# Performance work log

Hardware: AMD Instinct MI355X
Metric: run time of the kernel (lower is better)

Reference implementation:

```python
import jax, jax.numpy as jnp
import numpy as np
from jax import lax

EPS = 1e-5
NF, NH, HD = 1024, 2, 2  # num_features, heads, head_size (hidden_size=4)


def _prelu(x, a):
    return jnp.where(x >= 0, x, a * x)


def _bn2d(x, g, b):  # training-mode BatchNorm2d over (N,H,W)
    m = x.mean(axis=(0, 2, 3), keepdims=True)
    v = ((x - m) ** 2).mean(axis=(0, 2, 3), keepdims=True)
    return (x - m) / jnp.sqrt(v + EPS) * g[None, :, None, None] + b[None, :, None, None]


def _bn1d(x, g, b):  # training-mode BatchNorm1d over batch
    m = x.mean(axis=0, keepdims=True)
    v = ((x - m) ** 2).mean(axis=0, keepdims=True)
    return (x - m) / jnp.sqrt(v + EPS) * g + b


def _ln(x, g, b):
    m = x.mean(axis=-1, keepdims=True)
    v = ((x - m) ** 2).mean(axis=-1, keepdims=True)
    return (x - m) / jnp.sqrt(v + EPS) * g + b


def _conv(x, w, b, stride):
    y = lax.conv_general_dilated(x, w, window_strides=stride, padding='VALID',
                                 dimension_numbers=('NCHW', 'OIHW', 'NCHW'))
    return y + b[None, :, None, None]


def setup_inputs() -> dict:
    key = jax.random.key(0)
    ks = jax.random.split(key, 24)
    r = lambda i, shape, s=0.05: jax.random.normal(ks[i], shape, jnp.float32) * s
    ones = lambda n: jnp.ones((n,), jnp.float32)
    zeros = lambda n: jnp.zeros((n,), jnp.float32)
    return {
        'vertex_pos': r(0, (32, 3), 1.0),
        'body_mesh': r(1, (32, 20813, 3), 1.0),
        'conv1_w': r(2, (3, 1, 409, 3)), 'conv1_b': r(3, (3,)),
        'bn1_g': ones(3), 'bn1_b': zeros(3),
        'conv2_w': r(4, (3, 1, 330, 3)), 'conv2_b': r(5, (3,)),
        'bn2_g': ones(3), 'bn2_b': zeros(3),
        'prelu_a': jnp.float32(0.25),
        'wq': r(6, (4, 9)), 'bq': r(7, (4,)),
        'wk': r(8, (4, 9)), 'bk': r(9, (4,)),
        'wv': r(10, (4, 9)), 'bv': r(11, (4,)),
        'fc_w': r(12, (1024, 4096)), 'fc_b': r(13, (1024,)),
        'ff1_w': r(14, (1024, 1024)), 'ff1_b': r(15, (1024,)),
        'ln_g': ones(1024), 'ln_b': zeros(1024),
        'ff2_w': r(16, (48, 1024)), 'ff2_b': r(17, (48,)),
        'fus_w0': r(18, (48, 32, 3)), 'fus_b0': r(19, (48, 32)),
        'fus_w1': r(20, (48, 128, 32)), 'fus_b1': r(21, (48, 128)),
        'bnf0_g': ones(32), 'bnf0_b': zeros(32),
        'bnf1_g': ones(128), 'bnf1_b': zeros(128),
        'prelu_f': jnp.float32(0.25),
        'out_w': r(22, (1, 128)), 'out_b': r(23, (1,)),
    }


def reference(vertex_pos, body_mesh, conv1_w, conv1_b, bn1_g, bn1_b, conv2_w, conv2_b,
              bn2_g, bn2_b, prelu_a, wq, bq, wk, bk, wv, bv, fc_w, fc_b,
              ff1_w, ff1_b, ln_g, ln_b, ff2_w, ff2_b,
              fus_w0, fus_b0, fus_w1, fus_b1, bnf0_g, bnf0_b, bnf1_g, bnf1_b,
              prelu_f, out_w, out_b):
    B = vertex_pos.shape[0]
    # --- mesh encoder (MultiHeadAttention_conv.mesh_encoder) ---
    mesh = body_mesh.reshape(B, 1, -1, 3)                             # [B,1,20813,3]
    x = _bn2d(_conv(mesh, conv1_w, conv1_b, (6, 1)), bn1_g, bn1_b)    # [B,3,3401,1]
    x = x.reshape(B, 1, -1, 3)                                        # [B,1,3401,3]
    x = _bn2d(_conv(x, conv2_w, conv2_b, (1, 1)), bn2_g, bn2_b)       # [B,3,3072,1]
    x = _prelu(x.reshape(B, NF, -1), prelu_a)                         # [B,1024,9]
    # --- multi-head attention ---
    def heads(t):  # [B,NF,NH*HD] -> [B,NH,NF,HD]
        return t.reshape(B, NF, NH, HD).transpose(0, 2, 1, 3)
    q = heads(x @ wq.T + bq)
    k = heads(x @ wk.T + bk)
    v = heads(x @ wv.T + bv)
    scores = jnp.einsum('bhqd,bhkd->bhqk', q, k) / (HD ** 0.5)        # [B,2,1024,1024]
    attn = jax.nn.softmax(scores, axis=-1)
    av = jnp.einsum('bhqk,bhkd->bhqd', attn, v)
    av = av.transpose(0, 2, 1, 3).reshape(B, NF * NH * HD)            # [B,4096]
    h = av @ fc_w.T + fc_b                                            # [B,1024]
    # --- GMW feed-forward (residual) + motion weights ---
    h = h + jax.nn.elu(_ln(h @ ff1_w.T + ff1_b, ln_g, ln_b))
    mw = h @ ff2_w.T + ff2_b                                          # [B,48]
    w = mw / jnp.sum(mw, axis=1, keepdims=True)                       # normalized gates
    # --- fused MoE stage: 48 experts per depth, batched as one grouped GEMM ---
    s = vertex_pos.reshape(B, 3)
    for We, be, g, bb in ((fus_w0, fus_b0, bnf0_g, bnf0_b),
                          (fus_w1, fus_b1, bnf1_g, bnf1_b)):
        y = jnp.einsum('eoi,bi->beo', We, s) + be[None]               # [B,48,out]
        s = jnp.einsum('beo,be->bo', y, w)                            # gated sum over experts
        s = _prelu(_bn1d(s, g, bb), prelu_f)
    return jax.nn.sigmoid(s @ out_w.T + out_b)                        # [B,1]
```

## Files before the change

### kernel.cpp

```cpp
#include <hip/hip_runtime.h>

#define EPSF 1e-5f

__device__ __forceinline__ float wred(float v) {
#pragma unroll
  for (int off = 32; off > 0; off >>= 1) v += __shfl_down(v, off, 64);
  return v;
}

__global__ __launch_bounds__(256) void k_conv1(
    const float* __restrict__ mesh, const float* __restrict__ cw,
    const float* __restrict__ cb, float* __restrict__ out,
    float* __restrict__ part) {
  __shared__ float wsm[3684];
  __shared__ float sm[3513];
  __shared__ float red[3072];
  __shared__ float pm2[384];
  __shared__ float redm[4][6];
  const int tid = threadIdx.x;
  const int tile = blockIdx.x % 27, b = blockIdx.x / 27;
  const int oh0 = tile << 7;
  const int nvalid = min(128, 3401 - oh0);
  const int nload = (nvalid - 1) * 18 + 1227;
  for (int j = tid; j < 3681; j += 256) {
    int c = (j >= 2454) ? 2 : ((j >= 1227) ? 1 : 0);
    wsm[c * 1228 + (j - c * 1227)] = cw[j];
  }
  const float* src = mesh + b * 62439 + oh0 * 18;
  for (int j = tid; j < nload; j += 256) sm[j] = src[j];
  __syncthreads();
  const int kc = tid >> 5, s = tid & 31;
  const int i0 = kc * 154, i1 = min(1227, i0 + 154);
  float acc[4][3] = {};
  const float* xb = sm + s * 18;
  int i = i0;
#pragma unroll 2
  for (; i + 1 < i1; i += 2) {
    float2 w0 = *(const float2*)(wsm + i);
    float2 w1 = *(const float2*)(wsm + 1228 + i);
    float2 w2 = *(const float2*)(wsm + 2456 + i);
#pragma unroll
    for (int r = 0; r < 4; ++r) {
      float2 x = *(const float2*)(xb + r * 576 + i);
      acc[r][0] = fmaf(w0.x, x.x, fmaf(w0.y, x.y, acc[r][0]));
      acc[r][1] = fmaf(w1.x, x.x, fmaf(w1.y, x.y, acc[r][1]));
      acc[r][2] = fmaf(w2.x, x.x, fmaf(w2.y, x.y, acc[r][2]));
    }
  }
  if (i < i1) {
    float w0 = wsm[i], w1 = wsm[1228 + i], w2 = wsm[2456 + i];
#pragma unroll
    for (int r = 0; r < 4; ++r) {
      float x = xb[r * 576 + i];
      acc[r][0] = fmaf(w0, x, acc[r][0]);
      acc[r][1] = fmaf(w1, x, acc[r][1]);
      acc[r][2] = fmaf(w2, x, acc[r][2]);
    }
  }
#pragma unroll
  for (int r = 0; r < 4; ++r)
#pragma unroll
    for (int ch = 0; ch < 3; ++ch)
      red[kc * 384 + s * 12 + r * 3 + ch] = acc[r][ch];
  __syncthreads();
  float v0 = cb[tid % 3];
#pragma unroll
  for (int c2 = 0; c2 < 8; ++c2) v0 += red[c2 * 384 + tid];
  pm2[tid] = v0;
  if (tid < 128) {
    float v1 = cb[(tid + 256) % 3];
#pragma unroll
    for (int c2 = 0; c2 < 8; ++c2) v1 += red[c2 * 384 + tid + 256];
    pm2[tid + 256] = v1;
  }
  __syncthreads();
  float st[6] = {0.f, 0.f, 0.f, 0.f, 0.f, 0.f};
  if (tid < 128 && tid < nvalid) {
    const int s2 = tid & 31, r2 = tid >> 5;
    float y0 = pm2[s2 * 12 + r2 * 3 + 0];
    float y1 = pm2[s2 * 12 + r2 * 3 + 1];
    float y2 = pm2[s2 * 12 + r2 * 3 + 2];
    float* op = out + b * 10203 + oh0 + tid;
    op[0] = y0; op[3401] = y1; op[6802] = y2;
    st[0] = y0; st[1] = y0 * y0; st[2] = y1; st[3] = y1 * y1; st[4] = y2; st[5] = y2 * y2;
  }
  const int lane = tid & 63, wid = tid >> 6;
#pragma unroll
  for (int c = 0; c < 6; ++c) {
    float rv = wred(st[c]);
    if (lane == 0) redm[wid][c] = rv;
  }
  __syncthreads();
  if (tid < 6)
    part[tid * 864 + blockIdx.x] = redm[0][tid] + redm[1][tid] + redm[2][tid] + redm[3][tid];
}

__global__ __launch_bounds__(256) void k_conv2(
    const float* __restrict__ x1, const float* __restrict__ part1,
    const float* __restrict__ g1, const float* __restrict__ be1,
    const float* __restrict__ cw, const float* __restrict__ cb,
    float* __restrict__ out, float* __restrict__ part) {
  __shared__ float wT[3024];
  __shared__ float P[3][852];
  __shared__ float red[1536];
  __shared__ float redm[4][6];
  __shared__ float coef[6];
  const int tid = threadIdx.x;
  const int lane = tid & 63, wid = tid >> 6;
  {
    float r6[6] = {0.f, 0.f, 0.f, 0.f, 0.f, 0.f};
    for (int j = tid; j < 864; j += 256) {
#pragma unroll
      for (int c = 0; c < 6; ++c) r6[c] += part1[c * 864 + j];
    }
#pragma unroll
    for (int c = 0; c < 6; ++c) {
      float rv = wred(r6[c]);
      if (lane == 0) redm[wid][c] = rv;
    }
    __syncthreads();
    if (tid == 0) {
      const float inv_n = 1.f / (32.f * 3401.f);
#pragma unroll
      for (int c = 0; c < 3; ++c) {
        float s = redm[0][2 * c] + redm[1][2 * c] + redm[2][2 * c] + redm[3][2 * c];
        float ss = redm[0][2 * c + 1] + redm[1][2 * c + 1] + redm[2][2 * c + 1] + redm[3][2 * c + 1];
        float m = s * inv_n;
        float var = ss * inv_n - m * m;
        float a = g1[c] * rsqrtf(var + EPSF);
        coef[c] = a; coef[3 + c] = be1[c] - m * a;
      }
    }
  }
  for (int j = tid; j < 3024; j += 256) {
    int u = j / 1008, rem = j - u * 1008;
    int c = rem / 336, t = rem - c * 336;
    wT[j] = (t < 330) ? cw[c * 990 + 3 * t + u] : 0.f;
  }
  __syncthreads();
  const int tile = blockIdx.x % 6, b = blockIdx.x / 6;
  const int oh0 = tile << 9;
  const int zbase = oh0 * 3;
  const float* src = x1 + b * 10203 + zbase;
  for (int j = tid; j < 2556; j += 256) {
    int rel = j / 3, u = j - rel * 3;
    float val = 0.f;
    int z = zbase + j;
    if (z <= 10202) {
      int c = (z >= 6802) ? 2 : ((z >= 3401) ? 1 : 0);
      val = fmaf(coef[c], src[j], coef[3 + c]);
    }
    P[u][rel] = val;
  }
  __syncthreads();
  const int kc = tid >> 7, s = tid & 127;
  const int t0 = kc * 168;
  const int xb = s << 2;
  float acc0[4] = {}, acc1[4] = {}, acc2[4] = {};
  float4 cur0 = *(const float4*)&P[0][xb + t0];
  float4 cur1 = *(const float4*)&P[1][xb + t0];
  float4 cur2 = *(const float4*)&P[2][xb + t0];
  float4 nxt0 = *(const float4*)&P[0][xb + t0 + 4];
  float4 nxt1 = *(const float4*)&P[1][xb + t0 + 4];
  float4 nxt2 = *(const float4*)&P[2][xb + t0 + 4];
  const int tend = t0 + 168;
  for (int tg = t0; tg < tend; tg += 4) {
#define CONV2_U(ACC0, ACC1, ACC2, UOFF, CUR, NXT)                                                  \
    {                                                                                              \
      const float* wu = wT + UOFF + tg;                                                            \
      float2 wa0 = *(const float2*)(wu);                                                           \
      float2 wb0 = *(const float2*)(wu + 2);                                                       \
      float2 wa1 = *(const float2*)(wu + 336);                                                     \
      float2 wb1 = *(const float2*)(wu + 338);                                                     \
      float2 wa2 = *(const float2*)(wu + 672);                                                     \
      float2 wb2 = *(const float2*)(wu + 674);                                                     \
      float x0 = CUR.x, x1v = CUR.y, x2v = CUR.z, x3v = CUR.w;                                     \
      float x4 = NXT.x, x5 = NXT.y, x6 = NXT.z;                                                    \
      ACC0[0] = fmaf(wa0.x, x0,  fmaf(wa0.y, x1v, fmaf(wb0.x, x2v, fmaf(wb0.y, x3v, ACC0[0]))));  \
      ACC0[1] = fmaf(wa0.x, x1v, fmaf(wa0.y, x2v, fmaf(wb0.x, x3v, fmaf(wb0.y, x4,  ACC0[1]))));  \
      ACC0[2] = fmaf(wa0.x, x2v, fmaf(wa0.y, x3v, fmaf(wb0.x, x4,  fmaf(wb0.y, x5,  ACC0[2]))));  \
      ACC0[3] = fmaf(wa0.x, x3v, fmaf(wa0.y, x4,  fmaf(wb0.x, x5,  fmaf(wb0.y, x6,  ACC0[3]))));  \
      ACC1[0] = fmaf(wa1.x, x0,  fmaf(wa1.y, x1v, fmaf(wb1.x, x2v, fmaf(wb1.y, x3v, ACC1[0]))));  \
      ACC1[1] = fmaf(wa1.x, x1v, fmaf(wa1.y, x2v, fmaf(wb1.x, x3v, fmaf(wb1.y, x4,  ACC1[1]))));  \
      ACC1[2] = fmaf(wa1.x, x2v, fmaf(wa1.y, x3v, fmaf(wb1.x, x4,  fmaf(wb1.y, x5,  ACC1[2]))));  \
      ACC1[3] = fmaf(wa1.x, x3v, fmaf(wa1.y, x4,  fmaf(wb1.x, x5,  fmaf(wb1.y, x6,  ACC1[3]))));  \
      ACC2[0] = fmaf(wa2.x, x0,  fmaf(wa2.y, x1v, fmaf(wb2.x, x2v, fmaf(wb2.y, x3v, ACC2[0]))));  \
      ACC2[1] = fmaf(wa2.x, x1v, fmaf(wa2.y, x2v, fmaf(wb2.x, x3v, fmaf(wb2.y, x4,  ACC2[1]))));  \
      ACC2[2] = fmaf(wa2.x, x2v, fmaf(wa2.y, x3v, fmaf(wb2.x, x4,  fmaf(wb2.y, x5,  ACC2[2]))));  \
      ACC2[3] = fmaf(wa2.x, x3v, fmaf(wa2.y, x4,  fmaf(wb2.x, x5,  fmaf(wb2.y, x6,  ACC2[3]))));  \
    }
    CONV2_U(acc0, acc1, acc2, 0,    cur0, nxt0)
    CONV2_U(acc0, acc1, acc2, 1008, cur1, nxt1)
    CONV2_U(acc0, acc1, acc2, 2016, cur2, nxt2)
#undef CONV2_U
    cur0 = nxt0; cur1 = nxt1; cur2 = nxt2;
    nxt0 = *(const float4*)&P[0][xb + tg + 8];
    nxt1 = *(const float4*)&P[1][xb + tg + 8];
    nxt2 = *(const float4*)&P[2][xb + tg + 8];
  }
  if (kc == 1) {
#pragma unroll
    for (int r = 0; r < 4; ++r) {
      red[s * 12 + r] = acc0[r];
      red[s * 12 + 4 + r] = acc1[r];
      red[s * 12 + 8 + r] = acc2[r];
    }
  }
  __syncthreads();
  float st[6] = {0.f, 0.f, 0.f, 0.f, 0.f, 0.f};
  if (kc == 0) {
    float y0[4], y1[4], y2[4];
#pragma unroll
    for (int r = 0; r < 4; ++r) {
      y0[r] = acc0[r] + red[s * 12 + r] + cb[0];
      y1[r] = acc1[r] + red[s * 12 + 4 + r] + cb[1];
      y2[r] = acc2[r] + red[s * 12 + 8 + r] + cb[2];
      st[0] += y0[r]; st[1] += y0[r] * y0[r];
      st[2] += y1[r]; st[3] += y1[r] * y1[r];
      st[4] += y2[r]; st[5] += y2[r] * y2[r];
    }
    float* op = out + b * 9216 + oh0 + xb;
    *(float4*)(op)        = make_float4(y0[0], y0[1], y0[2], y0[3]);
    *(float4*)(op + 3072) = make_float4(y1[0], y1[1], y1[2], y1[3]);
    *(float4*)(op + 6144) = make_float4(y2[0], y2[1], y2[2], y2[3]);
  }
#pragma unroll
  for (int c = 0; c < 6; ++c) {
    float rv = wred(st[c]);
    if (lane == 0) redm[wid][c] = rv;
  }
  __syncthreads();
  if (tid < 6)
    part[tid * 192 + blockIdx.x] = redm[0][tid] + redm[1][tid] + redm[2][tid] + redm[3][tid];
}

__global__ __launch_bounds__(256) void k_qkv(
    const float* __restrict__ x2, const float* __restrict__ part2,
    const float* __restrict__ g2, const float* __restrict__ be2,
    const float* __restrict__ pa_p,
    const float* __restrict__ wq, const float* __restrict__ bq,
    const float* __restrict__ wk, const float* __restrict__ bk,
    const float* __restrict__ wv, const float* __restrict__ bv,
    float* __restrict__ qo, float* __restrict__ ko, float* __restrict__ vo) {
  __shared__ float redm[4][6];
  __shared__ float coef[6];
  const int tid = threadIdx.x;
  const int lane = tid & 63, wid = tid >> 6;
  {
    float r[6] = {0.f, 0.f, 0.f, 0.f, 0.f, 0.f};
    for (int j = tid; j < 192; j += 256) {
#pragma unroll
      for (int c = 0; c < 6; ++c) r[c] += part2[c * 192 + j];
    }
#pragma unroll
    for (int c = 0; c < 6; ++c) {
      float rv = wred(r[c]);
      if (lane == 0) redm[wid][c] = rv;
    }
    __syncthreads();
    if (tid == 0) {
      const float inv_n = 1.f / (32.f * 3072.f);
#pragma unroll
      for (int c = 0; c < 3; ++c) {
        float s = redm[0][2 * c] + redm[1][2 * c] + redm[2][2 * c] + redm[3][2 * c];
        float ss = redm[0][2 * c + 1] + redm[1][2 * c + 1] + redm[2][2 * c + 1] + redm[3][2 * c + 1];
        float m = s * inv_n;
        float var = ss * inv_n - m * m;
        float a = g2[c] * rsqrtf(var + EPSF);
        coef[c] = a; coef[3 + c] = be2[c] - m * a;
      }
    }
    __syncthreads();
  }
  const float pa = pa_p[0];
  const int id = blockIdx.x * 256 + tid;
  const int b = id >> 10, f = id & 1023;
  const float* src = x2 + b * 9216 + f * 9;
  float x[9];
  const int z0 = f * 9;
#pragma unroll
  for (int j = 0; j < 9; ++j) {
    int z = z0 + j;
    int c = (z >= 6144) ? 2 : ((z >= 3072) ? 1 : 0);
    float v = fmaf(coef[c], src[j], coef[3 + c]);
    x[j] = (v >= 0.f) ? v : pa * v;
  }
  const float QSCALE = 0.70710678118654752f * 1.44269504088896341f;
#pragma unroll
  for (int dd = 0; dd < 4; ++dd) {
    float q = bq[dd], k = bk[dd], v = bv[dd];
#pragma unroll
    for (int j = 0; j < 9; ++j) {
      q = fmaf(wq[dd * 9 + j], x[j], q);
      k = fmaf(wk[dd * 9 + j], x[j], k);
      v = fmaf(wv[dd * 9 + j], x[j], v);
    }
    int hh = dd >> 1, d = dd & 1;
    int idx = ((b * 2 + hh) * 1024 + f) * 2 + d;
    qo[idx] = q * QSCALE;
    ko[idx] = k;
    vo[idx] = v;
  }
}

__device__ __forceinline__ int kvIdx(int j) { return j + (j >> 7); }

__global__ __launch_bounds__(256) void k_attn(
    const float* __restrict__ q, const float* __restrict__ k,
    const float* __restrict__ v, float* __restrict__ av) {
  __shared__ float4 kv[1032];
  __shared__ float smax[4];
  const int tid = threadIdx.x;
  const int bh = blockIdx.x >> 3, rblk = blockIdx.x & 7;
  const float2* kp = (const float2*)(k + bh * 2048);
  const float2* vp = (const float2*)(v + bh * 2048);
  float nkm = 0.f;
  for (int j = tid; j < 1024; j += 256) {
    float2 kk = kp[j], vv = vp[j];
    kv[kvIdx(j)] = make_float4(kk.x, kk.y, vv.x, vv.y);
    nkm = fmaxf(nkm, fmaf(kk.x, kk.x, kk.y * kk.y));
  }
#pragma unroll
  for (int off = 32; off > 0; off >>= 1) nkm = fmaxf(nkm, __shfl_xor(nkm, off, 64));
  if ((tid & 63) == 0) smax[tid >> 6] = nkm;
  __syncthreads();
  const float knorm = sqrtf(fmaxf(fmaxf(smax[0], smax[1]), fmaxf(smax[2], smax[3])));
  const int lane = tid & 63, w = tid >> 6;
  const int rg = (w << 3) | (lane >> 3);
  const int ks = lane & 7;
  const int r0 = rblk * 128 + rg * 4;
  const float4 q01 = *(const float4*)(q + (bh * 1024 + r0) * 2);
  const float4 q23 = *(const float4*)(q + (bh * 1024 + r0) * 2 + 4);
  float qx[4] = {q01.x, q01.z, q23.x, q23.z};
  float qy[4] = {q01.y, q01.w, q23.y, q23.w};
  float m[4], l[4] = {0.f, 0.f, 0.f, 0.f};
  float o0[4] = {0.f, 0.f, 0.f, 0.f}, o1[4] = {0.f, 0.f, 0.f, 0.f};
#pragma unroll
  for (int r = 0; r < 4; ++r) m[r] = sqrtf(fmaf(qx[r], qx[r], qy[r] * qy[r])) * knorm;
  const int j0 = ks * 128;
#pragma unroll 4
  for (int jj = 0; jj < 128; ++jj) {
    float4 kk = kv[kvIdx(j0 + jj)];
#pragma unroll
    for (int r = 0; r < 4; ++r) {
      float s = fmaf(qx[r], kk.x, qy[r] * kk.y);
      float p = exp2f(s - m[r]);
      l[r] += p;
      o0[r] = fmaf(p, kk.z, o0[r]);
      o1[r] = fmaf(p, kk.w, o1[r]);
    }
  }
#pragma unroll
  for (int off = 1; off <= 4; off <<= 1) {
#pragma unroll
    for (int r = 0; r < 4; ++r) {
      l[r] += __shfl_xor(l[r], off, 64);
      o0[r] += __shfl_xor(o0[r], off, 64);
      o1[r] += __shfl_xor(o1[r], off, 64);
    }
  }
  if (ks == 0) {
    const int b = bh >> 1, hh = bh & 1;
#pragma unroll
    for (int r = 0; r < 4; ++r) {
      float rl = 1.f / l[r];
      *(float2*)(av + b * 4096 + (r0 + r) * 4 + hh * 2) = make_float2(o0[r] * rl, o1[r] * rl);
    }
  }
}

__global__ __launch_bounds__(256) void k_fc(
    const float* __restrict__ x, const float* __restrict__ w,
    float* __restrict__ pout) {
  __shared__ float xs[128 * 36];
  const int tid = threadIdx.x;
  const int ob = blockIdx.x & 15, ksp = blockIdx.x >> 4;
  const int k0 = ksp * 128, obase = ob * 64;
  for (int r = tid; r < 4096; r += 256) {
    int b = r >> 7, kk = r & 127;
    xs[kk * 36 + b] = x[b * 4096 + k0 + kk];
  }
  __syncthreads();
  const int og = tid & 15, bg = tid >> 4;
  const int o = obase + og * 4, bb0 = bg * 2;
  float acc[4][2] = {};
  const float* wp = w + o * 4096 + k0;
  for (int kk = 0; kk < 128; kk += 4) {
    float2 x0 = *(const float2*)&xs[(kk + 0) * 36 + bb0];
    float2 x1 = *(const float2*)&xs[(kk + 1) * 36 + bb0];
    float2 x2 = *(const float2*)&xs[(kk + 2) * 36 + bb0];
    float2 x3 = *(const float2*)&xs[(kk + 3) * 36 + bb0];
#pragma unroll
    for (int oo = 0; oo < 4; ++oo) {
      float4 wv = *(const float4*)(wp + oo * 4096 + kk);
      acc[oo][0] = fmaf(wv.x, x0.x, fmaf(wv.y, x1.x, fmaf(wv.z, x2.x, fmaf(wv.w, x3.x, acc[oo][0]))));
      acc[oo][1] = fmaf(wv.x, x0.y, fmaf(wv.y, x1.y, fmaf(wv.z, x2.y, fmaf(wv.w, x3.y, acc[oo][1]))));
    }
  }
#pragma unroll
  for (int bi = 0; bi < 2; ++bi) {
    float4 rv = make_float4(acc[0][bi], acc[1][bi], acc[2][bi], acc[3][bi]);
    *(float4*)&pout[(ksp * 32 + bb0 + bi) * 1024 + o] = rv;
  }
}

__global__ __launch_bounds__(256) void k_hred(
    const float* __restrict__ pfc, const float* __restrict__ fcb,
    float* __restrict__ h) {
  const int idx = blockIdx.x * 256 + threadIdx.x;
  const int b = idx >> 10, o = idx & 1023;
  float hv = fcb[o];
#pragma unroll 4
  for (int j = 0; j < 32; ++j) hv += pfc[(j * 32 + b) * 1024 + o];
  h[idx] = hv;
}

__global__ __launch_bounds__(256) void k_ff1(
    const float* __restrict__ h, const float* __restrict__ w,
    float* __restrict__ pout) {
  __shared__ float xs[64 * 36];
  const int tid = threadIdx.x;
  const int ob = blockIdx.x & 15, ksp = blockIdx.x >> 4;
  const int k0 = ksp * 64, obase = ob * 64;
  for (int r = tid; r < 2048; r += 256) {
    int b = r >> 6, kk = r & 63;
    xs[kk * 36 + b] = h[b * 1024 + k0 + kk];
  }
  __syncthreads();
  const int og = tid & 15, bg = tid >> 4;
  const int o = obase + og * 4, bb0 = bg * 2;
  float acc[4][2] = {};
  const float* wp = w + o * 1024 + k0;
  for (int kk = 0; kk < 64; kk += 4) {
    float2 x0 = *(const float2*)&xs[(kk + 0) * 36 + bb0];
    float2 x1 = *(const float2*)&xs[(kk + 1) * 36 + bb0];
    float2 x2 = *(const float2*)&xs[(kk + 2) * 36 + bb0];
    float2 x3 = *(const float2*)&xs[(kk + 3) * 36 + bb0];
#pragma unroll
    for (int oo = 0; oo < 4; ++oo) {
      float4 wv = *(const float4*)(wp + oo * 1024 + kk);
      acc[oo][0] = fmaf(wv.x, x0.x, fmaf(wv.y, x1.x, fmaf(wv.z, x2.x, fmaf(wv.w, x3.x, acc[oo][0]))));
      acc[oo][1] = fmaf(wv.x, x0.y, fmaf(wv.y, x1.y, fmaf(wv.z, x2.y, fmaf(wv.w, x3.y, acc[oo][1]))));
    }
  }
#pragma unroll
  for (int bi = 0; bi < 2; ++bi) {
    float4 rv = make_float4(acc[0][bi], acc[1][bi], acc[2][bi], acc[3][bi]);
    *(float4*)&pout[(ksp * 32 + bb0 + bi) * 1024 + o] = rv;
  }
}

__global__ __launch_bounds__(256) void k_tail1(
    const float* __restrict__ h, const float* __restrict__ pff1,
    const float* __restrict__ ff1b,
    const float* __restrict__ lng, const float* __restrict__ lnb,
    const float* __restrict__ f2w, const float* __restrict__ f2b,
    const float* __restrict__ vp, const float* __restrict__ w0,
    const float* __restrict__ b0, float* __restrict__ wgate,
    float* __restrict__ s1pre) {
  __shared__ float hs[1024], ts[1024];
  __shared__ float mw_s[48];
  __shared__ float red2[4][2];
  __shared__ float bc[2];
  __shared__ float tot_s;
  const int b = blockIdx.x, tid = threadIdx.x;
  const int lane = tid & 63, wid = tid >> 6;
  for (int o = tid; o < 1024; o += 256) {
    hs[o] = h[b * 1024 + o];
    float tv = ff1b[o];
#pragma unroll 4
    for (int j = 0; j < 16; ++j) tv += pff1[(j * 32 + b) * 1024 + o];
    ts[o] = tv;
  }
  __syncthreads();
  float ls = 0.f, lss = 0.f;
  for (int o = tid; o < 1024; o += 256) {
    float t = ts[o];
    ls += t; lss += t * t;
  }
  ls = wred(ls); lss = wred(lss);
  if (lane == 0) { red2[wid][0] = ls; red2[wid][1] = lss; }
  __syncthreads();
  if (tid == 0) {
    float S = red2[0][0] + red2[1][0] + red2[2][0] + red2[3][0];
    float SS = red2[0][1] + red2[1][1] + red2[2][1] + red2[3][1];
    float m = S * (1.f / 1024.f);
    float var = SS * (1.f / 1024.f) - m * m;
    bc[0] = m; bc[1] = rsqrtf(var + EPSF);
  }
  __syncthreads();
  const float m = bc[0], inv = bc[1];
  for (int o = tid; o < 1024; o += 256) {
    float y = fmaf((ts[o] - m) * inv, lng[o], lnb[o]);
    float e = (y > 0.f) ? y : expm1f(y);
    ts[o] = hs[o] + e;
  }
  __syncthreads();
  if (tid < 192) {
    int e = tid >> 2, part = tid & 3;
    float acc = 0.f;
    const float* wr = f2w + e * 1024 + part * 4;
    for (int i = 0; i < 64; ++i) {
      float4 wv = *(const float4*)(wr + i * 16);
      int ob = i * 16 + part * 4;
      acc = fmaf(wv.x, ts[ob], fmaf(wv.y, ts[ob + 1], fmaf(wv.z, ts[ob + 2], fmaf(wv.w, ts[ob + 3], acc))));
    }
    acc += __shfl_down(acc, 1, 64);
    acc += __shfl_down(acc, 2, 64);
    if (part == 0) mw_s[e] = acc + f2b[e];
  }
  __syncthreads();
  if (tid < 64) {
    float v = (tid < 48) ? mw_s[tid] : 0.f;
    float t = wred(v);
    if (tid == 0) tot_s = t;
  }
  __syncthreads();
  if (tid < 48) {
    float wg = mw_s[tid] / tot_s;
    mw_s[tid] = wg;
    wgate[b * 48 + tid] = wg;
  }
  __syncthreads();
  if (tid < 32) {
    const int o = tid;
    const float v0 = vp[b * 3], v1 = vp[b * 3 + 1], v2 = vp[b * 3 + 2];
    float acc = 0.f;
#pragma unroll 4
    for (int e = 0; e < 48; ++e) {
      const float* wr = w0 + (e * 32 + o) * 3;
      float y = b0[e * 32 + o] + wr[0] * v0 + wr[1] * v1 + wr[2] * v2;
      acc = fmaf(mw_s[e], y, acc);
    }
    s1pre[b * 32 + o] = acc;
  }
}

__global__ __launch_bounds__(128) void k_moe1(
    const float* __restrict__ s1pre, const float* __restrict__ g0,
    const float* __restrict__ be0, const float* __restrict__ pf_p,
    const float* __restrict__ wgate, const float* __restrict__ w1,
    const float* __restrict__ b1, float* __restrict__ pmoe) {
  __shared__ float s1n[32];
  __shared__ float wgs[6];
  const int tid = threadIdx.x;
  const int b = blockIdx.x >> 3, ech = blockIdx.x & 7;
  const int e0 = ech * 6;
  const float pf = pf_p[0];
  if (tid < 6) wgs[tid] = wgate[b * 48 + e0 + tid];
  if (tid < 32) {
    const int o = tid;
    float s = 0.f, ss = 0.f;
    for (int bb = 0; bb < 32; ++bb) {
      float v = s1pre[bb * 32 + o];
      s += v; ss += v * v;
    }
    float mm = s * (1.f / 32.f);
    float var = ss * (1.f / 32.f) - mm * mm;
    float a = g0[o] * rsqrtf(var + EPSF);
    float c = be0[o] - mm * a;
    float v = fmaf(s1pre[b * 32 + o], a, c);
    s1n[o] = (v >= 0.f) ? v : pf * v;
  }
  __syncthreads();
  const int op = tid;
  float acc = 0.f;
#pragma unroll
  for (int ee = 0; ee < 6; ++ee) {
    const int e = e0 + ee;
    const float* wr = w1 + (e * 128 + op) * 32;
    float y = b1[e * 128 + op];
#pragma unroll
    for (int i = 0; i < 32; i += 4) {
      float4 wv = *(const float4*)(wr + i);
      y = fmaf(wv.x, s1n[i], fmaf(wv.y, s1n[i + 1], fmaf(wv.z, s1n[i + 2], fmaf(wv.w, s1n[i + 3], y))));
    }
    acc = fmaf(wgs[ee], y, acc);
  }
  pmoe[ech * 4096 + b * 128 + op] = acc;
}

__global__ __launch_bounds__(256) void k_final(
    const float* __restrict__ pmoe, const float* __restrict__ g1,
    const float* __restrict__ be1, const float* __restrict__ pf_p,
    const float* __restrict__ ow, const float* __restrict__ obp,
    float* __restrict__ outp) {
  __shared__ float s2[32 * 132];
  __shared__ float ca[128], cb[128];
  const int tid = threadIdx.x;
  for (int r = tid; r < 4096; r += 256) {
    int b = r >> 7, o = r & 127;
    float v = 0.f;
#pragma unroll
    for (int j = 0; j < 8; ++j) v += pmoe[j * 4096 + r];
    s2[b * 132 + o] = v;
  }
  __syncthreads();
  if (tid < 128) {
    const int o = tid;
    float s = 0.f, ss = 0.f;
    for (int b = 0; b < 32; ++b) {
      float v = s2[b * 132 + o];
      s += v; ss += v * v;
    }
    float mm = s * (1.f / 32.f);
    float var = ss * (1.f / 32.f) - mm * mm;
    float a = g1[o] * rsqrtf(var + EPSF);
    ca[o] = a; cb[o] = be1[o] - mm * a;
  }
  __syncthreads();
  const float pf = pf_p[0];
  if (tid < 32) {
    const int b = tid;
    float acc = 0.f;
#pragma unroll 4
    for (int o = 0; o < 128; ++o) {
      float v = fmaf(s2[b * 132 + o], ca[o], cb[o]);
      v = (v >= 0.f) ? v : pf * v;
      acc = fmaf(v, ow[o], acc);
    }
    float z = acc + obp[0];
    outp[b] = 1.f / (1.f + __expf(-z));
  }
}

extern "C" void kernel_launch(void* const* d_in, const int* in_sizes, int n_in,
                              void* d_out, int out_size, void* d_ws, size_t ws_size,
                              hipStream_t stream) {
  (void)in_sizes; (void)n_in; (void)out_size; (void)ws_size;
  const float* vertex_pos = (const float*)d_in[0];
  const float* body_mesh  = (const float*)d_in[1];
  const float* conv1_w    = (const float*)d_in[2];
  const float* conv1_b    = (const float*)d_in[3];
  const float* bn1_g      = (const float*)d_in[4];
  const float* bn1_b      = (const float*)d_in[5];
  const float* conv2_w    = (const float*)d_in[6];
  const float* conv2_b    = (const float*)d_in[7];
  const float* bn2_g      = (const float*)d_in[8];
  const float* bn2_b      = (const float*)d_in[9];
  const float* prelu_a    = (const float*)d_in[10];
  const float* wq = (const float*)d_in[11]; const float* bq = (const float*)d_in[12];
  const float* wk = (const float*)d_in[13]; const float* bk = (const float*)d_in[14];
  const float* wv = (const float*)d_in[15]; const float* bv = (const float*)d_in[16];
  const float* fc_w  = (const float*)d_in[17]; const float* fc_b  = (const float*)d_in[18];
  const float* ff1_w = (const float*)d_in[19]; const float* ff1_b = (const float*)d_in[20];
  const float* ln_g  = (const float*)d_in[21]; const float* ln_b  = (const float*)d_in[22];
  const float* ff2_w = (const float*)d_in[23]; const float* ff2_b = (const float*)d_in[24];
  const float* fus_w0 = (const float*)d_in[25]; const float* fus_b0 = (const float*)d_in[26];
  const float* fus_w1 = (const float*)d_in[27]; const float* fus_b1 = (const float*)d_in[28];
  const float* bnf0_g = (const float*)d_in[29]; const float* bnf0_b = (const float*)d_in[30];
  const float* bnf1_g = (const float*)d_in[31]; const float* bnf1_b = (const float*)d_in[32];
  const float* prelu_f = (const float*)d_in[33];
  const float* out_w = (const float*)d_in[34]; const float* out_b = (const float*)d_in[35];

  float* ws = (float*)d_ws;
  float* conv1_out = ws + 0;
  float* conv2_out = ws + 326496;
  float* qws = ws + 621408;
  float* kws = ws + 752480;
  float* vws = ws + 883552;
  float* p_fc = ws + 0;
  float* av    = ws + 1048576;
  float* hbuf  = ws + 1179648;
  float* p_ff1 = ws + 1212416;
  float* part1 = ws + 1736704;
  float* part2 = ws + 1741888;
  float* wgate = ws + 1746496;
  float* s1pre = ws + 1748032;
  float* pmoe  = ws + 1749056;

  k_conv1<<<864, 256, 0, stream>>>(body_mesh, conv1_w, conv1_b, conv1_out, part1);
  k_conv2<<<192, 256, 0, stream>>>(conv1_out, part1, bn1_g, bn1_b, conv2_w, conv2_b, conv2_out, part2);
  k_qkv<<<128, 256, 0, stream>>>(conv2_out, part2, bn2_g, bn2_b, prelu_a,
                                 wq, bq, wk, bk, wv, bv, qws, kws, vws);
  k_attn<<<512, 256, 0, stream>>>(qws, kws, vws, av);
  k_fc<<<512, 256, 0, stream>>>(av, fc_w, p_fc);
  k_hred<<<128, 256, 0, stream>>>(p_fc, fc_b, hbuf);
  k_ff1<<<256, 256, 0, stream>>>(hbuf, ff1_w, p_ff1);
  k_tail1<<<32, 256, 0, stream>>>(hbuf, p_ff1, ff1_b, ln_g, ln_b, ff2_w, ff2_b,
                                  vertex_pos, fus_w0, fus_b0, wgate, s1pre);
  k_moe1<<<256, 128, 0, stream>>>(s1pre, bnf0_g, bnf0_b, prelu_f, wgate, fus_w1, fus_b1, pmoe);
  k_final<<<1, 256, 0, stream>>>(pmoe, bnf1_g, bnf1_b, prelu_f, out_w, out_b, (float*)d_out);
}
```

Measured before the change: 325.0 us.

## Restructure conv1 as stride-phase decomposition with register-reused sliding inputs

Rewrites the first convolution kernel so that inputs and weights are stored in shared memory split by stride phase (u = i mod 18). Each thread now computes 4 consecutive outputs and reuses a sliding float4 window of inputs across those outputs and the 3 channels, which cuts shared-memory loads per FMA. The mapping of threads to outputs changes to contiguous groups of 4, and the final output indexing is updated to match. The cost is padded shared arrays, integer division in the load phase, and some zero-padded work on the tail.

```diff
diff --git a/kernel.cpp b/kernel.cpp
--- a/kernel.cpp
+++ b/kernel.cpp
@@ -12,8 +12,8 @@
     const float* __restrict__ mesh, const float* __restrict__ cw,
     const float* __restrict__ cb, float* __restrict__ out,
     float* __restrict__ part) {
-  __shared__ float wsm[3684];
-  __shared__ float sm[3513];
+  __shared__ float wT[3888];
+  __shared__ float P[3672];
   __shared__ float red[3072];
   __shared__ float pm2[384];
   __shared__ float redm[4][6];
@@ -21,47 +21,62 @@
   const int tile = blockIdx.x % 27, b = blockIdx.x / 27;
   const int oh0 = tile << 7;
   const int nvalid = min(128, 3401 - oh0);
-  const int nload = (nvalid - 1) * 18 + 1227;
-  for (int j = tid; j < 3681; j += 256) {
-    int c = (j >= 2454) ? 2 : ((j >= 1227) ? 1 : 0);
-    wsm[c * 1228 + (j - c * 1227)] = cw[j];
-  }
-  const float* src = mesh + b * 62439 + oh0 * 18;
-  for (int j = tid; j < nload; j += 256) sm[j] = src[j];
+  for (int j = tid; j < 3888; j += 256) {
+    int c = j / 1296, rem = j - c * 1296;
+    int u = rem / 72, t = rem - u * 72;
+    int i = 18 * t + u;
+    wT[j] = (i < 1227) ? cw[c * 1227 + i] : 0.f;
+  }
+  {
+    const int zoff = oh0 * 18;
+    const float* src = mesh + b * 62439;
+    for (int j = tid; j < 3672; j += 256) {
+      int p = j / 18, u = j - p * 18;
+      int z = zoff + j;
+      P[u * 204 + p] = (z < 62439) ? src[z] : 0.f;
+    }
+  }
   __syncthreads();
   const int kc = tid >> 5, s = tid & 31;
-  const int i0 = kc * 154, i1 = min(1227, i0 + 154);
-  float acc[4][3] = {};
-  const float* xb = sm + s * 18;
-  int i = i0;
-#pragma unroll 2
-  for (; i + 1 < i1; i += 2) {
-    float2 w0 = *(const float2*)(wsm + i);
-    float2 w1 = *(const float2*)(wsm + 1228 + i);
-    float2 w2 = *(const float2*)(wsm + 2456 + i);
-#pragma unroll
-    for (int r = 0; r < 4; ++r) {
-      float2 x = *(const float2*)(xb + r * 576 + i);
-      acc[r][0] = fmaf(w0.x, x.x, fmaf(w0.y, x.y, acc[r][0]));
-      acc[r][1] = fmaf(w1.x, x.x, fmaf(w1.y, x.y, acc[r][1]));
-      acc[r][2] = fmaf(w2.x, x.x, fmaf(w2.y, x.y, acc[r][2]));
-    }
-  }
-  if (i < i1) {
-    float w0 = wsm[i], w1 = wsm[1228 + i], w2 = wsm[2456 + i];
-#pragma unroll
-    for (int r = 0; r < 4; ++r) {
-      float x = xb[r * 576 + i];
-      acc[r][0] = fmaf(w0, x, acc[r][0]);
-      acc[r][1] = fmaf(w1, x, acc[r][1]);
-      acc[r][2] = fmaf(w2, x, acc[r][2]);
+  const int xb = s << 2;
+  const int nu = (kc < 2) ? 3 : 2;
+  float acc[3][4] = {};
+  for (int ui = 0; ui < nu; ++ui) {
+    const int u = (ui == 0) ? kc : ((ui == 1) ? kc + 8 : kc + 16);
+    const float* Pu = P + u * 204 + xb;
+    const float* w0p = wT + u * 72;
+    const float* w1p = wT + 1296 + u * 72;
+    const float* w2p = wT + 2592 + u * 72;
+    float4 cur = *(const float4*)(Pu);
+    float4 nxt = *(const float4*)(Pu + 4);
+#pragma unroll 6
+    for (int tg = 0; tg < 72; tg += 4) {
+      float4 wv0 = *(const float4*)(w0p + tg);
+      float4 wv1 = *(const float4*)(w1p + tg);
+      float4 wv2 = *(const float4*)(w2p + tg);
+      float x0 = cur.x, x1 = cur.y, x2 = cur.z, x3 = cur.w;
+      float x4 = nxt.x, x5 = nxt.y, x6 = nxt.z;
+      acc[0][0] = fmaf(wv0.x, x0, fmaf(wv0.y, x1, fmaf(wv0.z, x2, fmaf(wv0.w, x3, acc[0][0]))));
+      acc[0][1] = fmaf(wv0.x, x1, fmaf(wv0.y, x2, fmaf(wv0.z, x3, fmaf(wv0.w, x4, acc[0][1]))));
+      acc[0][2] = fmaf(wv0.x, x2, fmaf(wv0.y, x3, fmaf(wv0.z, x4, fmaf(wv0.w, x5, acc[0][2]))));
+      acc[0][3] = fmaf(wv0.x, x3, fmaf(wv0.y, x4, fmaf(wv0.z, x5, fmaf(wv0.w, x6, acc[0][3]))));
+      acc[1][0] = fmaf(wv1.x, x0, fmaf(wv1.y, x1, fmaf(wv1.z, x2, fmaf(wv1.w, x3, acc[1][0]))));
+      acc[1][1] = fmaf(wv1.x, x1, fmaf(wv1.y, x2, fmaf(wv1.z, x3, fmaf(wv1.w, x4, acc[1][1]))));
+      acc[1][2] = fmaf(wv1.x, x2, fmaf(wv1.y, x3, fmaf(wv1.z, x4, fmaf(wv1.w, x5, acc[1][2]))));
+      acc[1][3] = fmaf(wv1.x, x3, fmaf(wv1.y, x4, fmaf(wv1.z, x5, fmaf(wv1.w, x6, acc[1][3]))));
+      acc[2][0] = fmaf(wv2.x, x0, fmaf(wv2.y, x1, fmaf(wv2.z, x2, fmaf(wv2.w, x3, acc[2][0]))));
+      acc[2][1] = fmaf(wv2.x, x1, fmaf(wv2.y, x2, fmaf(wv2.z, x3, fmaf(wv2.w, x4, acc[2][1]))));
+      acc[2][2] = fmaf(wv2.x, x2, fmaf(wv2.y, x3, fmaf(wv2.z, x4, fmaf(wv2.w, x5, acc[2][2]))));
+      acc[2][3] = fmaf(wv2.x, x3, fmaf(wv2.y, x4, fmaf(wv2.z, x5, fmaf(wv2.w, x6, acc[2][3]))));
+      cur = nxt;
+      nxt = *(const float4*)(Pu + tg + 8);
     }
   }
 #pragma unroll
   for (int r = 0; r < 4; ++r)
 #pragma unroll
     for (int ch = 0; ch < 3; ++ch)
-      red[kc * 384 + s * 12 + r * 3 + ch] = acc[r][ch];
+      red[kc * 384 + s * 12 + r * 3 + ch] = acc[ch][r];
   __syncthreads();
   float v0 = cb[tid % 3];
 #pragma unroll
@@ -75,8 +90,8 @@
   }
   __syncthreads();
   float st[6] = {0.f, 0.f, 0.f, 0.f, 0.f, 0.f};
-  if (tid < 128 && tid < nvalid) {
-    const int s2 = tid & 31, r2 = tid >> 5;
+  if (tid < nvalid) {
+    const int s2 = tid >> 2, r2 = tid & 3;
     float y0 = pm2[s2 * 12 + r2 * 3 + 0];
     float y1 = pm2[s2 * 12 + r2 * 3 + 1];
     float y2 = pm2[s2 * 12 + r2 * 3 + 2];
```

New measurement: 323.8 us. About the same (-0.4%).
